# Optimization experiments

Hardware: AMD Instinct MI355X
Metric: run time of the kernel (lower is better)

## Reference

```python
import jax, jax.numpy as jnp
import numpy as np

HEADS = 8
NEG_SLOPE = 0.2  # PyG GATConv default LeakyReLU slope


def _gat_layer(x, src, dst, W, a_src, a_dst, bias, heads, out_ch):
    """PyG-style GATConv (concat heads, self-loops already appended, eval mode).
    x: [N, F_in]; src/dst: [E_tot] int; W: [F_in, heads*out_ch];
    a_src/a_dst: [heads, out_ch]; bias: [heads*out_ch].
    """
    N = x.shape[0]
    h = (x @ W).reshape(N, heads, out_ch)                      # [N, H, C]
    # per-node attention logits (gathered per edge as scalars, not features)
    al_s = jnp.einsum('nhc,hc->nh', h, a_src)                  # [N, H]
    al_d = jnp.einsum('nhc,hc->nh', h, a_dst)                  # [N, H]
    e = jax.nn.leaky_relu(al_s[src] + al_d[dst], negative_slope=NEG_SLOPE)  # [E, H]
    # segment softmax over incoming edges of each target node (stable)
    e_max = jax.ops.segment_max(e, dst, num_segments=N)        # self-loops => no empty segments
    ex = jnp.exp(e - e_max[dst])
    denom = jax.ops.segment_sum(ex, dst, num_segments=N)
    alpha = ex / (denom[dst] + 1e-16)                          # [E, H]
    # gather source features, weight, scatter-add to targets
    out = jax.ops.segment_sum(h[src] * alpha[:, :, None], dst, num_segments=N)  # [N, H, C]
    return out.reshape(N, heads * out_ch) + bias


def setup_inputs() -> dict:
    key = jax.random.key(0)
    ks = jax.random.split(key, 16)
    N, E, F_IN, NUM_CLASSES = 50000, 1600000, 128, 16
    s = 0.1
    return {
        'x': jax.random.normal(ks[0], (N, F_IN), dtype=jnp.float32),
        'edge_index': jax.random.randint(ks[1], (2, E), 0, N, dtype=jnp.int64),
        # GAT layer 1: 128 -> 8 heads x 8
        'W1': jax.random.normal(ks[2], (F_IN, 64), dtype=jnp.float32) * s,
        'a1_src': jax.random.normal(ks[3], (8, 8), dtype=jnp.float32) * s,
        'a1_dst': jax.random.normal(ks[4], (8, 8), dtype=jnp.float32) * s,
        'b1': jnp.zeros((64,), dtype=jnp.float32),
        # GAT layer 2: 64 -> 8 heads x 4
        'W2': jax.random.normal(ks[5], (64, 32), dtype=jnp.float32) * s,
        'a2_src': jax.random.normal(ks[6], (8, 4), dtype=jnp.float32) * s,
        'a2_dst': jax.random.normal(ks[7], (8, 4), dtype=jnp.float32) * s,
        'b2': jnp.zeros((32,), dtype=jnp.float32),
        # torch MultiheadAttention(32, 8): packed in_proj [96,32], out_proj [32,32]
        'in_proj_w': jax.random.normal(ks[8], (96, 32), dtype=jnp.float32) * s,
        'in_proj_b': jnp.zeros((96,), dtype=jnp.float32),
        'out_proj_w': jax.random.normal(ks[9], (32, 32), dtype=jnp.float32) * s,
        'out_proj_b': jnp.zeros((32,), dtype=jnp.float32),
        # fc: 32 -> num_classes
        'fc_w': jax.random.normal(ks[10], (NUM_CLASSES, 32), dtype=jnp.float32) * s,
        'fc_b': jnp.zeros((NUM_CLASSES,), dtype=jnp.float32),
    }


def reference(x, edge_index, W1, a1_src, a1_dst, b1, W2, a2_src, a2_dst, b2,
              in_proj_w, in_proj_b, out_proj_w, out_proj_b, fc_w, fc_b):
    N = x.shape[0]
    loops = jnp.arange(N, dtype=edge_index.dtype)
    src = jnp.concatenate([edge_index[0], loops])  # PyG add_self_loops=True
    dst = jnp.concatenate([edge_index[1], loops])

    h = jax.nn.elu(_gat_layer(x, src, dst, W1, a1_src, a1_dst, b1, HEADS, 8))   # [N, 64]
    h = jax.nn.elu(_gat_layer(h, src, dst, W2, a2_src, a2_dst, b2, HEADS, 4))   # [N, 32]

    # MultiheadAttention on h.unsqueeze(0): shape [1, N, 32] with torch's
    # seq-first layout => seq_len = 1, batch = N. Softmax over a single key
    # is identically 1 for every head, so out = out_proj(v_proj(h)).
    v = h @ in_proj_w[64:96].T + in_proj_b[64:96]   # v-projection slice of packed in_proj
    h = v @ out_proj_w.T + out_proj_b               # [N, 32]

    logits = h @ fc_w.T + fc_b                      # [N, num_classes]
    return jax.nn.log_softmax(logits, axis=1)
```

## Files before the change

kernel.cpp:

```cpp
#include <hip/hip_runtime.h>
#include <hip/hip_bf16.h>
#include <math.h>


#define BSHIFT 7
#define BMASK  ((1 << BSHIFT) - 1)
#define MAXNB  512
#define TILE   8192
#define XST    136
#define SMBYTES 36864

typedef __attribute__((ext_vector_type(8))) short short8;
typedef __attribute__((ext_vector_type(4))) float floatx4;
typedef __attribute__((ext_vector_type(2))) float floatx2;

__device__ __forceinline__ unsigned short f2bf(float f) {
    union { float f; unsigned int u; } v; v.f = f;
    unsigned int u = v.u;
    return (unsigned short)((u + 0x7FFFu + ((u >> 16) & 1u)) >> 16);
}
__device__ __forceinline__ float lrelu(float e) { return fmaxf(e, 0.2f * e); }
__device__ __forceinline__ float elu(float o) {
    return (o > 0.f) ? o : (__expf(o) - 1.f);
}

__global__ __launch_bounds__(256) void fused_pre_kernel(
    const float* __restrict__ x, const float* __restrict__ W,
    const float* __restrict__ a_src, const float* __restrict__ a_dst,
    char* __restrict__ rec1, float* __restrict__ ald, int N, int GB,
    const int* __restrict__ ei, int E, int Et, int NB, int CAP,
    int* __restrict__ gcount, unsigned int* __restrict__ rec, int NT,
    const float* __restrict__ in_proj_w, const float* __restrict__ in_proj_b,
    const float* __restrict__ out_proj_w, const float* __restrict__ out_proj_b,
    const float* __restrict__ fc_w, const float* __restrict__ fc_b,
    float* __restrict__ M, float* __restrict__ bf) {
    __shared__ __align__(16) char sm[SMBYTES];
    int t = threadIdx.x;
    int bid = blockIdx.x;
    if (bid < GB) {
        unsigned short* xs = (unsigned short*)sm;
        unsigned short* wt = xs + 64 * XST;
        int nb = bid * 64;
#pragma unroll
        for (int r = 0; r < 8; ++r) {
            int p = t + 256 * r;
            int row = p >> 5;
            int c4  = p & 31;
            int n = nb + row;
            float4 v = (n < N) ? ((const float4*)x)[(size_t)n * 32 + c4]
                               : make_float4(0.f, 0.f, 0.f, 0.f);
            unsigned short* dst = &xs[row * XST + c4 * 4];
            dst[0] = f2bf(v.x); dst[1] = f2bf(v.y);
            dst[2] = f2bf(v.z); dst[3] = f2bf(v.w);
        }
        {
            int n = t & 63, kg = t >> 6;
#pragma unroll
            for (int c = 0; c < 4; ++c) {
                int k0 = kg * 32 + c * 8;
                unsigned short* dst = &wt[n * XST + k0];
#pragma unroll
                for (int j = 0; j < 8; ++j)
                    dst[j] = f2bf(W[(k0 + j) * 64 + n]);
            }
        }
        __syncthreads();
        int wave = t >> 6, lane = t & 63;
        int m16 = lane & 15, quad = lane >> 4;
        floatx4 acc[4];
#pragma unroll
        for (int i = 0; i < 4; ++i) acc[i] = (floatx4){0.f, 0.f, 0.f, 0.f};
#pragma unroll
        for (int k = 0; k < 4; ++k) {
            int koff = k * 32 + quad * 8;
            short8 afrag = *(const short8*)&xs[(wave * 16 + m16) * XST + koff];
#pragma unroll
            for (int nt = 0; nt < 4; ++nt) {
                short8 bfrag = *(const short8*)&wt[(nt * 16 + m16) * XST + koff];
                acc[nt] = __builtin_amdgcn_mfma_f32_16x16x32_bf16(afrag, bfrag, acc[nt], 0, 0, 0);
            }
        }
        __syncthreads();
        float* hs = (float*)sm;
#pragma unroll
        for (int nt = 0; nt < 4; ++nt)
#pragma unroll
            for (int r = 0; r < 4; ++r)
                hs[(wave * 16 + quad * 4 + r) * 65 + nt * 16 + m16] = acc[nt][r];
        __syncthreads();
        float asv = a_src[lane], adv = a_dst[lane];
        for (int itn = 0; itn < 16; ++itn) {
            int nl = wave * 16 + itn;
            int n = nb + nl;
            if (n >= N) break;
            float v = hs[nl * 65 + lane];
            float ps = v * asv, pd = v * adv;
            ps += __shfl_xor(ps, 1); ps += __shfl_xor(ps, 2); ps += __shfl_xor(ps, 4);
            pd += __shfl_xor(pd, 1); pd += __shfl_xor(pd, 2); pd += __shfl_xor(pd, 4);
            if ((lane & 7) == 0) {
                *(float*)(rec1 + (size_t)n * 128 + 4 * (lane >> 3)) = ps;
                ald[n * 8 + (lane >> 3)] = pd;
            }
            if (lane < 16) {
                const float* hr = &hs[nl * 65 + lane * 4];
                int pk = __builtin_amdgcn_cvt_pk_fp8_f32(hr[0], hr[1], 0, false);
                pk = __builtin_amdgcn_cvt_pk_fp8_f32(hr[2], hr[3], pk, true);
                *(unsigned*)(rec1 + (size_t)n * 128 + 64 + 4 * lane) = (unsigned)pk;
            }
        }
    } else if (bid < GB + NT) {
        unsigned int* lrec = (unsigned int*)sm;
        int* h   = (int*)(sm + TILE * 4);
        int* cur = (int*)(sm + TILE * 4 + MAXNB * 4);
        for (int i = t; i < NB; i += 256) h[i] = 0;
        int tile0 = (bid - GB) * TILE;
        int cnt = Et - tile0; if (cnt > TILE) cnt = TILE;
        __syncthreads();
        for (int j = t; j < cnt; j += 256) {
            int jj = tile0 + j;
            int srcv, d;
            if (jj < E) { srcv = ei[jj]; d = ei[E + jj]; } else { srcv = jj - E; d = jj - E; }
            lrec[j] = (unsigned)srcv | ((unsigned)d << 16);
            atomicAdd(&h[d >> BSHIFT], 1);
        }
        __syncthreads();
        for (int i = t; i < NB; i += 256)
            cur[i] = h[i] ? atomicAdd(&gcount[i], h[i]) : 0;
        __syncthreads();
        for (int j = t; j < cnt; j += 256) {
            unsigned v = lrec[j];
            int b = v >> (16 + BSHIFT);
            int pos = atomicAdd(&cur[b], 1);
            if (pos < CAP)
                rec[(size_t)b * CAP + pos] =
                    (v & 0xFFFFu) | ((((v >> 16) & BMASK)) << 16);
        }
    } else {
        float* Wvo = (float*)sm;
        float* bvo = (float*)(sm + 4096);
        const float* Wv = in_proj_w + 64 * 32;
        const float* bv = in_proj_b + 64;
        for (int idx = t; idx < 1024; idx += 256) {
            int i = idx >> 5, j = idx & 31;
            float acc = 0.f;
            for (int k = 0; k < 32; ++k) acc += out_proj_w[i * 32 + k] * Wv[k * 32 + j];
            Wvo[idx] = acc;
        }
        if (t < 32) {
            float acc = 0.f;
            for (int k = 0; k < 32; ++k) acc += out_proj_w[t * 32 + k] * bv[k];
            bvo[t] = acc + out_proj_b[t];
        }
        __syncthreads();
        for (int idx = t; idx < 16 * 32; idx += 256) {
            int cc = idx >> 5, j = idx & 31;
            float acc = 0.f;
            for (int i = 0; i < 32; ++i) acc += fc_w[cc * 32 + i] * Wvo[i * 32 + j];
            M[idx] = acc;
        }
        if (t < 16) {
            float acc = 0.f;
            for (int i = 0; i < 32; ++i) acc += fc_w[t * 32 + i] * bvo[i];
            bf[t] = acc + fc_b[t];
        }
    }
}

__global__ __launch_bounds__(256) void csr_finalize_kernel(
    const unsigned int* __restrict__ rec, const int* __restrict__ gcount,
    int* __restrict__ rowp, unsigned short* __restrict__ esrc,
    int N, int Et, int CAP) {
    __shared__ int h[128];
    __shared__ int nb[128];
    __shared__ int cur[128];
    __shared__ int ssum[256];
    int b = blockIdx.x, t = threadIdx.x;
    size_t rbase = (size_t)b * CAP;
    int cnt = gcount[b]; if (cnt > CAP) cnt = CAP;
    if (t < 128) h[t] = 0;
    int acc = 0;
    for (int i = t; i < b; i += 256) {
        int v = gcount[i];
        acc += (v < CAP) ? v : CAP;
    }
    ssum[t] = acc;
    __syncthreads();
    for (int off = 128; off >= 1; off >>= 1) {
        if (t < off) ssum[t] += ssum[t + off];
        __syncthreads();
    }
    int obase = ssum[0];
    for (int i = t; i < cnt; i += 256)
        atomicAdd(&h[(rec[rbase + i] >> 16) & 127], 1);
    __syncthreads();
    if (t == 0) {
        int run = obase;
        for (int i = 0; i < 128; ++i) { nb[i] = run; run += h[i]; }
    }
    __syncthreads();
    if (t < 128) cur[t] = nb[t];
    int n0 = b << BSHIFT;
    if (t < 128 && n0 + t < N) rowp[n0 + t] = nb[t];
    if (b == 0 && t == 0) rowp[N] = Et;
    __syncthreads();
    for (int i = t; i < cnt; i += 256) {
        unsigned r = rec[rbase + i];
        int pos = atomicAdd(&cur[(r >> 16) & 127], 1);
        esrc[pos] = (unsigned short)(r & 0xFFFFu);
    }
}

__global__ __launch_bounds__(256) void gat_agg64_g2_kernel(
    const int* __restrict__ rowp, const unsigned short* __restrict__ esrc,
    const char* __restrict__ rec1, const float* __restrict__ ald_arr,
    const float* __restrict__ bias,
    const float* __restrict__ W2, const float* __restrict__ a2s,
    const float* __restrict__ a2d,
    char* __restrict__ rec2, float* __restrict__ ald2, int N) {
    __shared__ __align__(16) float W2p[2][8][32][4];
    __shared__ __align__(16) float oL[4][64];
    __shared__ __align__(16) float h2L[4][32];
    int t = threadIdx.x;
    for (int idx = t; idx < 2048; idx += 256) {
        int k = idx >> 5, l = idx & 31;
        W2p[k >> 5][(k & 31) >> 2][l][k & 3] = W2[idx];
    }
    __syncthreads();
    const int lane = t & 63;
    const int wv = t >> 6;
    const int e = lane >> 4;
    const int c = lane & 15;
    const int hd = c >> 1;
    const int aoff = 4 * hd;
    const int foff = 64 + 4 * c;
    int n = blockIdx.x * 4 + wv;
    if (n >= N) return;
    float aldv = ald_arr[n * 8 + hd];
    int beg = rowp[n], end = rowp[n + 1];
    float dA = 0.f, dB = 0.f;
    floatx2 p0a = {0.f, 0.f}, p0b = {0.f, 0.f};
    floatx2 p1a = {0.f, 0.f}, p1b = {0.f, 0.f};
    floatx2 p2a = {0.f, 0.f}, p2b = {0.f, 0.f};
    floatx2 p3a = {0.f, 0.f}, p3b = {0.f, 0.f};
    int i = beg;
    for (; i + 32 <= end; i += 32) {
        int s0 = esrc[i + e],      s1 = esrc[i + 4 + e];
        int s2 = esrc[i + 8 + e],  s3 = esrc[i + 12 + e];
        int s4 = esrc[i + 16 + e], s5 = esrc[i + 20 + e];
        int s6 = esrc[i + 24 + e], s7 = esrc[i + 28 + e];
        const char* r0 = rec1 + (size_t)s0 * 128;
        const char* r1 = rec1 + (size_t)s1 * 128;
        const char* r2 = rec1 + (size_t)s2 * 128;
        const char* r3 = rec1 + (size_t)s3 * 128;
        const char* r4 = rec1 + (size_t)s4 * 128;
        const char* r5 = rec1 + (size_t)s5 * 128;
        const char* r6 = rec1 + (size_t)s6 * 128;
        const char* r7 = rec1 + (size_t)s7 * 128;
        float e0 = *(const float*)(r0 + aoff), e1 = *(const float*)(r1 + aoff);
        float e2 = *(const float*)(r2 + aoff), e3 = *(const float*)(r3 + aoff);
        float e4 = *(const float*)(r4 + aoff), e5 = *(const float*)(r5 + aoff);
        float e6 = *(const float*)(r6 + aoff), e7 = *(const float*)(r7 + aoff);
        unsigned g0 = *(const unsigned*)(r0 + foff), g1 = *(const unsigned*)(r1 + foff);
        unsigned g2 = *(const unsigned*)(r2 + foff), g3 = *(const unsigned*)(r3 + foff);
        unsigned g4 = *(const unsigned*)(r4 + foff), g5 = *(const unsigned*)(r5 + foff);
        unsigned g6 = *(const unsigned*)(r6 + foff), g7 = *(const unsigned*)(r7 + foff);
        float w0 = __expf(lrelu(e0 + aldv));
        float w1 = __expf(lrelu(e1 + aldv));
        float w2 = __expf(lrelu(e2 + aldv));
        float w3 = __expf(lrelu(e3 + aldv));
        float w4 = __expf(lrelu(e4 + aldv));
        float w5 = __expf(lrelu(e5 + aldv));
        float w6 = __expf(lrelu(e6 + aldv));
        float w7 = __expf(lrelu(e7 + aldv));
        dA += w0 + w2; dB += w1 + w3;
        dA += w4 + w6; dB += w5 + w7;
        p0a += w0 * __builtin_amdgcn_cvt_pk_f32_fp8(g0, false);
        p0b += w0 * __builtin_amdgcn_cvt_pk_f32_fp8(g0, true);
        p1a += w1 * __builtin_amdgcn_cvt_pk_f32_fp8(g1, false);
        p1b += w1 * __builtin_amdgcn_cvt_pk_f32_fp8(g1, true);
        p2a += w2 * __builtin_amdgcn_cvt_pk_f32_fp8(g2, false);
        p2b += w2 * __builtin_amdgcn_cvt_pk_f32_fp8(g2, true);
        p3a += w3 * __builtin_amdgcn_cvt_pk_f32_fp8(g3, false);
        p3b += w3 * __builtin_amdgcn_cvt_pk_f32_fp8(g3, true);
        p0a += w4 * __builtin_amdgcn_cvt_pk_f32_fp8(g4, false);
        p0b += w4 * __builtin_amdgcn_cvt_pk_f32_fp8(g4, true);
        p1a += w5 * __builtin_amdgcn_cvt_pk_f32_fp8(g5, false);
        p1b += w5 * __builtin_amdgcn_cvt_pk_f32_fp8(g5, true);
        p2a += w6 * __builtin_amdgcn_cvt_pk_f32_fp8(g6, false);
        p2b += w6 * __builtin_amdgcn_cvt_pk_f32_fp8(g6, true);
        p3a += w7 * __builtin_amdgcn_cvt_pk_f32_fp8(g7, false);
        p3b += w7 * __builtin_amdgcn_cvt_pk_f32_fp8(g7, true);
    }
    for (; i < end; i += 16) {
        int i0 = i + e, i1 = i + 4 + e, i2 = i + 8 + e, i3 = i + 12 + e;
        bool v0 = i0 < end, v1 = i1 < end, v2 = i2 < end, v3 = i3 < end;
        int c0 = v0 ? i0 : beg;
        int c1 = v1 ? i1 : beg;
        int c2 = v2 ? i2 : beg;
        int c3 = v3 ? i3 : beg;
        int s0 = esrc[c0], s1 = esrc[c1], s2 = esrc[c2], s3 = esrc[c3];
        const char* r0 = rec1 + (size_t)s0 * 128;
        const char* r1 = rec1 + (size_t)s1 * 128;
        const char* r2 = rec1 + (size_t)s2 * 128;
        const char* r3 = rec1 + (size_t)s3 * 128;
        float e0 = *(const float*)(r0 + aoff), e1 = *(const float*)(r1 + aoff);
        float e2 = *(const float*)(r2 + aoff), e3 = *(const float*)(r3 + aoff);
        unsigned g0 = *(const unsigned*)(r0 + foff), g1 = *(const unsigned*)(r1 + foff);
        unsigned g2 = *(const unsigned*)(r2 + foff), g3 = *(const unsigned*)(r3 + foff);
        float w0 = v0 ? __expf(lrelu(e0 + aldv)) : 0.f;
        float w1 = v1 ? __expf(lrelu(e1 + aldv)) : 0.f;
        float w2 = v2 ? __expf(lrelu(e2 + aldv)) : 0.f;
        float w3 = v3 ? __expf(lrelu(e3 + aldv)) : 0.f;
        dA += w0 + w2; dB += w1 + w3;
        p0a += w0 * __builtin_amdgcn_cvt_pk_f32_fp8(g0, false);
        p0b += w0 * __builtin_amdgcn_cvt_pk_f32_fp8(g0, true);
        p1a += w1 * __builtin_amdgcn_cvt_pk_f32_fp8(g1, false);
        p1b += w1 * __builtin_amdgcn_cvt_pk_f32_fp8(g1, true);
        p2a += w2 * __builtin_amdgcn_cvt_pk_f32_fp8(g2, false);
        p2b += w2 * __builtin_amdgcn_cvt_pk_f32_fp8(g2, true);
        p3a += w3 * __builtin_amdgcn_cvt_pk_f32_fp8(g3, false);
        p3b += w3 * __builtin_amdgcn_cvt_pk_f32_fp8(g3, true);
    }
    float d = dA + dB;
    floatx2 Pa = (p0a + p1a) + (p2a + p3a);
    floatx2 Pb = (p0b + p1b) + (p2b + p3b);
    float P0 = Pa.x, P1 = Pa.y, P2 = Pb.x, P3 = Pb.y;
    d  += __shfl_xor(d, 16);  d  += __shfl_xor(d, 32);
    P0 += __shfl_xor(P0, 16); P0 += __shfl_xor(P0, 32);
    P1 += __shfl_xor(P1, 16); P1 += __shfl_xor(P1, 32);
    P2 += __shfl_xor(P2, 16); P2 += __shfl_xor(P2, 32);
    P3 += __shfl_xor(P3, 16); P3 += __shfl_xor(P3, 32);
    float inv = 1.f / (d + 1e-16f);
    float4 bv = ((const float4*)bias)[c];
    float o0 = elu(P0 * inv + bv.x);
    float o1 = elu(P1 * inv + bv.y);
    float o2 = elu(P2 * inv + bv.z);
    float o3 = elu(P3 * inv + bv.w);
    if (lane < 16) *(float4*)&oL[wv][c * 4] = make_float4(o0, o1, o2, o3);
    const int l = lane & 31, kh = lane >> 5;
    const float* orow = &oL[wv][kh * 32];
    float a0 = 0.f, a1 = 0.f, a2 = 0.f, a3 = 0.f;
#pragma unroll
    for (int g = 0; g < 8; ++g) {
        float4 ov = *(const float4*)&orow[g * 4];
        float4 wv4 = *(const float4*)&W2p[kh][g][l][0];
        a0 += ov.x * wv4.x; a1 += ov.y * wv4.y;
        a2 += ov.z * wv4.z; a3 += ov.w * wv4.w;
    }
    float acc = (a0 + a1) + (a2 + a3);
    acc += __shfl_xor(acc, 32);
    float ps = acc * a2s[l], pd = acc * a2d[l];
    ps += __shfl_xor(ps, 1); ps += __shfl_xor(ps, 2);
    pd += __shfl_xor(pd, 1); pd += __shfl_xor(pd, 2);
    if (lane < 32) {
        h2L[wv][l] = acc;
        if ((l & 3) == 0) {
            *(float*)(rec2 + (size_t)n * 64 + 4 * (l >> 2)) = ps;
            ald2[n * 8 + (l >> 2)] = pd;
        }
    }
    if (lane < 8) {
        const float* hr = &h2L[wv][lane * 4];
        int pk = __builtin_amdgcn_cvt_pk_fp8_f32(hr[0], hr[1], 0, false);
        pk = __builtin_amdgcn_cvt_pk_fp8_f32(hr[2], hr[3], pk, true);
        *(unsigned*)(rec2 + (size_t)n * 64 + 32 + 4 * lane) = (unsigned)pk;
    }
}

__global__ __launch_bounds__(256) void gat_agg32_fin_kernel(
    const int* __restrict__ rowp, const unsigned short* __restrict__ esrc,
    const char* __restrict__ rec2, const float* __restrict__ ald_arr,
    const float* __restrict__ bias,
    const float* __restrict__ M, const float* __restrict__ bf,
    float* __restrict__ out, int N) {
    __shared__ __align__(16) float Mp[8][16][4];
    __shared__ float bfs[16];
    __shared__ __align__(16) float oL[4][32];
    int t = threadIdx.x;
    for (int i = t; i < 512; i += 256) {
        int j = i >> 5, k = i & 31;
        Mp[k >> 2][j][k & 3] = M[i];
    }
    if (t < 16) bfs[t] = bf[t];
    __syncthreads();
    const int lane = t & 63;
    const int wv = t >> 6;
    const int e = lane >> 3;
    const int c = lane & 7;
    const int aoff = 4 * c;
    const int foff = 32 + 4 * c;
    int n = blockIdx.x * 4 + wv;
    if (n >= N) return;
    float aldv = ald_arr[n * 8 + c];
    int beg = rowp[n], end = rowp[n + 1];
    float d0 = 0.f, d1 = 0.f, d2 = 0.f, d3 = 0.f;
    floatx2 p0a = {0.f, 0.f}, p0b = {0.f, 0.f};
    floatx2 p1a = {0.f, 0.f}, p1b = {0.f, 0.f};
    floatx2 p2a = {0.f, 0.f}, p2b = {0.f, 0.f};
    floatx2 p3a = {0.f, 0.f}, p3b = {0.f, 0.f};
    int base = beg;
    for (; base + 32 <= end; base += 32) {
        int s0 = esrc[base + e],      s1 = esrc[base + 8 + e];
        int s2 = esrc[base + 16 + e], s3 = esrc[base + 24 + e];
        const char* r0 = rec2 + (size_t)s0 * 64;
        const char* r1 = rec2 + (size_t)s1 * 64;
        const char* r2 = rec2 + (size_t)s2 * 64;
        const char* r3 = rec2 + (size_t)s3 * 64;
        float e0 = *(const float*)(r0 + aoff) + aldv;
        float e1 = *(const float*)(r1 + aoff) + aldv;
        float e2 = *(const float*)(r2 + aoff) + aldv;
        float e3 = *(const float*)(r3 + aoff) + aldv;
        unsigned g0 = *(const unsigned*)(r0 + foff);
        unsigned g1 = *(const unsigned*)(r1 + foff);
        unsigned g2 = *(const unsigned*)(r2 + foff);
        unsigned g3 = *(const unsigned*)(r3 + foff);
        float w0 = __expf(lrelu(e0));
        float w1 = __expf(lrelu(e1));
        float w2 = __expf(lrelu(e2));
        float w3 = __expf(lrelu(e3));
        d0 += w0; d1 += w1; d2 += w2; d3 += w3;
        p0a += w0 * __builtin_amdgcn_cvt_pk_f32_fp8(g0, false);
        p0b += w0 * __builtin_amdgcn_cvt_pk_f32_fp8(g0, true);
        p1a += w1 * __builtin_amdgcn_cvt_pk_f32_fp8(g1, false);
        p1b += w1 * __builtin_amdgcn_cvt_pk_f32_fp8(g1, true);
        p2a += w2 * __builtin_amdgcn_cvt_pk_f32_fp8(g2, false);
        p2b += w2 * __builtin_amdgcn_cvt_pk_f32_fp8(g2, true);
        p3a += w3 * __builtin_amdgcn_cvt_pk_f32_fp8(g3, false);
        p3b += w3 * __builtin_amdgcn_cvt_pk_f32_fp8(g3, true);
    }
    for (; base < end; base += 32) {
        int i0 = base + e;
        int i1 = base + 8 + e;
        int i2 = base + 16 + e;
        int i3 = base + 24 + e;
        bool v0 = i0 < end, v1 = i1 < end, v2 = i2 < end, v3 = i3 < end;
        int c0 = v0 ? i0 : beg;
        int c1 = v1 ? i1 : beg;
        int c2 = v2 ? i2 : beg;
        int c3 = v3 ? i3 : beg;
        int s0 = esrc[c0], s1 = esrc[c1], s2 = esrc[c2], s3 = esrc[c3];
        const char* r0 = rec2 + (size_t)s0 * 64;
        const char* r1 = rec2 + (size_t)s1 * 64;
        const char* r2 = rec2 + (size_t)s2 * 64;
        const char* r3 = rec2 + (size_t)s3 * 64;
        float e0 = *(const float*)(r0 + aoff) + aldv;
        float e1 = *(const float*)(r1 + aoff) + aldv;
        float e2 = *(const float*)(r2 + aoff) + aldv;
        float e3 = *(const float*)(r3 + aoff) + aldv;
        unsigned g0 = *(const unsigned*)(r0 + foff);
        unsigned g1 = *(const unsigned*)(r1 + foff);
        unsigned g2 = *(const unsigned*)(r2 + foff);
        unsigned g3 = *(const unsigned*)(r3 + foff);
        float w0 = v0 ? __expf(lrelu(e0)) : 0.f;
        float w1 = v1 ? __expf(lrelu(e1)) : 0.f;
        float w2 = v2 ? __expf(lrelu(e2)) : 0.f;
        float w3 = v3 ? __expf(lrelu(e3)) : 0.f;
        d0 += w0; d1 += w1; d2 += w2; d3 += w3;
        p0a += w0 * __builtin_amdgcn_cvt_pk_f32_fp8(g0, false);
        p0b += w0 * __builtin_amdgcn_cvt_pk_f32_fp8(g0, true);
        p1a += w1 * __builtin_amdgcn_cvt_pk_f32_fp8(g1, false);
        p1b += w1 * __builtin_amdgcn_cvt_pk_f32_fp8(g1, true);
        p2a += w2 * __builtin_amdgcn_cvt_pk_f32_fp8(g2, false);
        p2b += w2 * __builtin_amdgcn_cvt_pk_f32_fp8(g2, true);
        p3a += w3 * __builtin_amdgcn_cvt_pk_f32_fp8(g3, false);
        p3b += w3 * __builtin_amdgcn_cvt_pk_f32_fp8(g3, true);
    }
    float d = (d0 + d1) + (d2 + d3);
    floatx2 Pa = (p0a + p1a) + (p2a + p3a);
    floatx2 Pb = (p0b + p1b) + (p2b + p3b);
    float P0 = Pa.x, P1 = Pa.y, P2 = Pb.x, P3 = Pb.y;
    d  += __shfl_xor(d, 8);  d  += __shfl_xor(d, 16);  d  += __shfl_xor(d, 32);
    P0 += __shfl_xor(P0, 8); P0 += __shfl_xor(P0, 16); P0 += __shfl_xor(P0, 32);
    P1 += __shfl_xor(P1, 8); P1 += __shfl_xor(P1, 16); P1 += __shfl_xor(P1, 32);
    P2 += __shfl_xor(P2, 8); P2 += __shfl_xor(P2, 16); P2 += __shfl_xor(P2, 32);
    P3 += __shfl_xor(P3, 8); P3 += __shfl_xor(P3, 16); P3 += __shfl_xor(P3, 32);
    float inv = 1.f / (d + 1e-16f);
    float4 bv = ((const float4*)bias)[c];
    float o0 = elu(P0 * inv + bv.x);
    float o1 = elu(P1 * inv + bv.y);
    float o2 = elu(P2 * inv + bv.z);
    float o3 = elu(P3 * inv + bv.w);
    if (lane < 8) *(float4*)&oL[wv][c * 4] = make_float4(o0, o1, o2, o3);
    const int j = lane & 15;
    const float* orow = oL[wv];
    float a0 = 0.f, a1 = 0.f, a2 = 0.f, a3 = 0.f;
#pragma unroll
    for (int g = 0; g < 8; ++g) {
        float4 ov = *(const float4*)&orow[g * 4];
        float4 mv = *(const float4*)&Mp[g][j][0];
        a0 += ov.x * mv.x; a1 += ov.y * mv.y;
        a2 += ov.z * mv.z; a3 += ov.w * mv.w;
    }
    float logit = (a0 + a1) + (a2 + a3) + bfs[j];
    float mx = logit;
    mx = fmaxf(mx, __shfl_xor(mx, 1));
    mx = fmaxf(mx, __shfl_xor(mx, 2));
    mx = fmaxf(mx, __shfl_xor(mx, 4));
    mx = fmaxf(mx, __shfl_xor(mx, 8));
    float ex = __expf(logit - mx);
    float se = ex;
    se += __shfl_xor(se, 1);
    se += __shfl_xor(se, 2);
    se += __shfl_xor(se, 4);
    se += __shfl_xor(se, 8);
    float res = logit - (mx + __logf(se));
    if (lane < 16) out[(size_t)n * 16 + j] = res;
}

extern "C" void kernel_launch(void* const* d_in, const int* in_sizes, int n_in,
                              void* d_out, int out_size, void* d_ws, size_t ws_size,
                              hipStream_t stream) {
    const float* x   = (const float*)d_in[0];
    const int*   ei  = (const int*)d_in[1];
    const float* W1  = (const float*)d_in[2];
    const float* a1s = (const float*)d_in[3];
    const float* a1d = (const float*)d_in[4];
    const float* b1  = (const float*)d_in[5];
    const float* W2  = (const float*)d_in[6];
    const float* a2s = (const float*)d_in[7];
    const float* a2d = (const float*)d_in[8];
    const float* b2  = (const float*)d_in[9];
    const float* ipw = (const float*)d_in[10];
    const float* ipb = (const float*)d_in[11];
    const float* opw = (const float*)d_in[12];
    const float* opb = (const float*)d_in[13];
    const float* fcw = (const float*)d_in[14];
    const float* fcb = (const float*)d_in[15];
    float* out = (float*)d_out;

    int N = in_sizes[0] / 128;
    int E = in_sizes[1] / 2;
    int Et = E + N;
    int NB = (N + BMASK) >> BSHIFT;
    int NTILES = (Et + TILE - 1) / TILE;
    int GB = (N + 63) / 64;
    int CAP = Et / NB;
    CAP = CAP + CAP / 8 + 256;
    CAP = (CAP + 255) & ~255;

    char* ws = (char*)d_ws;
    size_t off = 0;
    auto alloc = [&](size_t bytes) -> void* {
        void* p = ws + off;
        off += bytes;
        off = (off + 255) & ~(size_t)255;
        return p;
    };
    int*   bcount = (int*)alloc(MAXNB * 4);
    unsigned int*   rec  = (unsigned int*)alloc((size_t)NB * CAP * 4);
    int*   rowp   = (int*)alloc((size_t)(N + 1) * 4);
    unsigned short* esrc = (unsigned short*)alloc((size_t)Et * 2);
    char* rec1   = (char*)alloc((size_t)N * 128);
    float* al1d  = (float*)alloc((size_t)N * 8 * 4);
    char* rec2   = (char*)alloc((size_t)N * 64);
    float* al2d  = (float*)alloc((size_t)N * 8 * 4);
    float* Mf    = (float*)alloc(512 * 4);
    float* bff   = (float*)alloc(16 * 4);
    (void)ws_size; (void)n_in; (void)out_size;

    hipMemsetAsync(bcount, 0, MAXNB * 4, stream);
    fused_pre_kernel<<<GB + NTILES + 1, 256, 0, stream>>>(
        x, W1, a1s, a1d, rec1, al1d, N, GB,
        ei, E, Et, NB, CAP, bcount, rec, NTILES,
        ipw, ipb, opw, opb, fcw, fcb, Mf, bff);
    csr_finalize_kernel<<<NB, 256, 0, stream>>>(rec, bcount, rowp, esrc, N, Et, CAP);

    gat_agg64_g2_kernel<<<(N + 3) / 4, 256, 0, stream>>>(
        rowp, esrc, rec1, al1d, b1, W2, a2s, a2d, rec2, al2d, N);
    gat_agg32_fin_kernel<<<(N + 3) / 4, 256, 0, stream>>>(
        rowp, esrc, rec2, al2d, b2, Mf, bff, out, N);
}
```

Before: 211.9 us.

## Stage CSR scatter in LDS and widen per-lane feature loads in layer-1 aggregation

The CSR finalize kernel now scatters each bucket's edge sources into a shared-memory buffer and then writes them to global memory contiguously, replacing random global scatter writes. CAP is clamped to the LDS buffer size, which could drop edges if a bucket overflows. The layer-1 aggregation kernel remaps lanes so each lane handles one full head (8 fp8 features via a 64-bit load) across 8 edge slots, instead of half a head across 4 slots. This gives fewer, wider gathers per edge and one attention exp per head-edge, at the cost of an extra shuffle stage and more accumulators.

```diff
diff --git a/kernel.cpp b/kernel.cpp
--- a/kernel.cpp
+++ b/kernel.cpp
@@ -9,6 +9,7 @@
 #define TILE   8192
 #define XST    136
 #define SMBYTES 36864
+#define LESRC_MAX 6144
 
 typedef __attribute__((ext_vector_type(8))) short short8;
 typedef __attribute__((ext_vector_type(4))) float floatx4;
@@ -174,6 +175,7 @@
     __shared__ int nb[128];
     __shared__ int cur[128];
     __shared__ int ssum[256];
+    __shared__ unsigned short lesrc[LESRC_MAX];
     int b = blockIdx.x, t = threadIdx.x;
     size_t rbase = (size_t)b * CAP;
     int cnt = gcount[b]; if (cnt > CAP) cnt = CAP;
@@ -194,20 +196,23 @@
         atomicAdd(&h[(rec[rbase + i] >> 16) & 127], 1);
     __syncthreads();
     if (t == 0) {
-        int run = obase;
+        int run = 0;
         for (int i = 0; i < 128; ++i) { nb[i] = run; run += h[i]; }
     }
     __syncthreads();
     if (t < 128) cur[t] = nb[t];
     int n0 = b << BSHIFT;
-    if (t < 128 && n0 + t < N) rowp[n0 + t] = nb[t];
+    if (t < 128 && n0 + t < N) rowp[n0 + t] = obase + nb[t];
     if (b == 0 && t == 0) rowp[N] = Et;
     __syncthreads();
     for (int i = t; i < cnt; i += 256) {
         unsigned r = rec[rbase + i];
         int pos = atomicAdd(&cur[(r >> 16) & 127], 1);
-        esrc[pos] = (unsigned short)(r & 0xFFFFu);
-    }
+        lesrc[pos] = (unsigned short)(r & 0xFFFFu);
+    }
+    __syncthreads();
+    for (int i = t; i < cnt; i += 256)
+        esrc[obase + i] = lesrc[i];
 }
 
 __global__ __launch_bounds__(256) void gat_agg64_g2_kernel(
@@ -228,71 +233,53 @@
     __syncthreads();
     const int lane = t & 63;
     const int wv = t >> 6;
-    const int e = lane >> 4;
-    const int c = lane & 15;
-    const int hd = c >> 1;
-    const int aoff = 4 * hd;
-    const int foff = 64 + 4 * c;
+    const int e = lane >> 3;
+    const int c = lane & 7;
+    const int aoff = 4 * c;
+    const int foff = 64 + 8 * c;
     int n = blockIdx.x * 4 + wv;
     if (n >= N) return;
-    float aldv = ald_arr[n * 8 + hd];
+    float aldv = ald_arr[n * 8 + c];
     int beg = rowp[n], end = rowp[n + 1];
     float dA = 0.f, dB = 0.f;
-    floatx2 p0a = {0.f, 0.f}, p0b = {0.f, 0.f};
-    floatx2 p1a = {0.f, 0.f}, p1b = {0.f, 0.f};
-    floatx2 p2a = {0.f, 0.f}, p2b = {0.f, 0.f};
-    floatx2 p3a = {0.f, 0.f}, p3b = {0.f, 0.f};
+    floatx2 A0 = {0.f, 0.f}, A1 = {0.f, 0.f}, A2 = {0.f, 0.f}, A3 = {0.f, 0.f};
+    floatx2 B0 = {0.f, 0.f}, B1 = {0.f, 0.f}, B2 = {0.f, 0.f}, B3 = {0.f, 0.f};
     int i = beg;
     for (; i + 32 <= end; i += 32) {
-        int s0 = esrc[i + e],      s1 = esrc[i + 4 + e];
-        int s2 = esrc[i + 8 + e],  s3 = esrc[i + 12 + e];
-        int s4 = esrc[i + 16 + e], s5 = esrc[i + 20 + e];
-        int s6 = esrc[i + 24 + e], s7 = esrc[i + 28 + e];
+        int s0 = esrc[i + e],      s1 = esrc[i + 8 + e];
+        int s2 = esrc[i + 16 + e], s3 = esrc[i + 24 + e];
         const char* r0 = rec1 + (size_t)s0 * 128;
         const char* r1 = rec1 + (size_t)s1 * 128;
         const char* r2 = rec1 + (size_t)s2 * 128;
         const char* r3 = rec1 + (size_t)s3 * 128;
-        const char* r4 = rec1 + (size_t)s4 * 128;
-        const char* r5 = rec1 + (size_t)s5 * 128;
-        const char* r6 = rec1 + (size_t)s6 * 128;
-        const char* r7 = rec1 + (size_t)s7 * 128;
         float e0 = *(const float*)(r0 + aoff), e1 = *(const float*)(r1 + aoff);
         float e2 = *(const float*)(r2 + aoff), e3 = *(const float*)(r3 + aoff);
-        float e4 = *(const float*)(r4 + aoff), e5 = *(const float*)(r5 + aoff);
-        float e6 = *(const float*)(r6 + aoff), e7 = *(const float*)(r7 + aoff);
-        unsigned g0 = *(const unsigned*)(r0 + foff), g1 = *(const unsigned*)(r1 + foff);
-        unsigned g2 = *(const unsigned*)(r2 + foff), g3 = *(const unsigned*)(r3 + foff);
-        unsigned g4 = *(const unsigned*)(r4 + foff), g5 = *(const unsigned*)(r5 + foff);
-        unsigned g6 = *(const unsigned*)(r6 + foff), g7 = *(const unsigned*)(r7 + foff);
+        uint2 g0 = *(const uint2*)(r0 + foff), g1 = *(const uint2*)(r1 + foff);
+        uint2 g2 = *(const uint2*)(r2 + foff), g3 = *(const uint2*)(r3 + foff);
         float w0 = __expf(lrelu(e0 + aldv));
         float w1 = __expf(lrelu(e1 + aldv));
         float w2 = __expf(lrelu(e2 + aldv));
         float w3 = __expf(lrelu(e3 + aldv));
-        float w4 = __expf(lrelu(e4 + aldv));
-        float w5 = __expf(lrelu(e5 + aldv));
-        float w6 = __expf(lrelu(e6 + aldv));
-        float w7 = __expf(lrelu(e7 + aldv));
         dA += w0 + w2; dB += w1 + w3;
-        dA += w4 + w6; dB += w5 + w7;
-        p0a += w0 * __builtin_amdgcn_cvt_pk_f32_fp8(g0, false);
-        p0b += w0 * __builtin_amdgcn_cvt_pk_f32_fp8(g0, true);
-        p1a += w1 * __builtin_amdgcn_cvt_pk_f32_fp8(g1, false);
-        p1b += w1 * __builtin_amdgcn_cvt_pk_f32_fp8(g1, true);
-        p2a += w2 * __builtin_amdgcn_cvt_pk_f32_fp8(g2, false);
-        p2b += w2 * __builtin_amdgcn_cvt_pk_f32_fp8(g2, true);
-        p3a += w3 * __builtin_amdgcn_cvt_pk_f32_fp8(g3, false);
-        p3b += w3 * __builtin_amdgcn_cvt_pk_f32_fp8(g3, true);
-        p0a += w4 * __builtin_amdgcn_cvt_pk_f32_fp8(g4, false);
-        p0b += w4 * __builtin_amdgcn_cvt_pk_f32_fp8(g4, true);
-        p1a += w5 * __builtin_amdgcn_cvt_pk_f32_fp8(g5, false);
-        p1b += w5 * __builtin_amdgcn_cvt_pk_f32_fp8(g5, true);
-        p2a += w6 * __builtin_amdgcn_cvt_pk_f32_fp8(g6, false);
-        p2b += w6 * __builtin_amdgcn_cvt_pk_f32_fp8(g6, true);
-        p3a += w7 * __builtin_amdgcn_cvt_pk_f32_fp8(g7, false);
-        p3b += w7 * __builtin_amdgcn_cvt_pk_f32_fp8(g7, true);
-    }
-    for (; i < end; i += 16) {
-        int i0 = i + e, i1 = i + 4 + e, i2 = i + 8 + e, i3 = i + 12 + e;
+        A0 += w0 * __builtin_amdgcn_cvt_pk_f32_fp8(g0.x, false);
+        A1 += w0 * __builtin_amdgcn_cvt_pk_f32_fp8(g0.x, true);
+        A2 += w0 * __builtin_amdgcn_cvt_pk_f32_fp8(g0.y, false);
+        A3 += w0 * __builtin_amdgcn_cvt_pk_f32_fp8(g0.y, true);
+        B0 += w1 * __builtin_amdgcn_cvt_pk_f32_fp8(g1.x, false);
+        B1 += w1 * __builtin_amdgcn_cvt_pk_f32_fp8(g1.x, true);
+        B2 += w1 * __builtin_amdgcn_cvt_pk_f32_fp8(g1.y, false);
+        B3 += w1 * __builtin_amdgcn_cvt_pk_f32_fp8(g1.y, true);
+        A0 += w2 * __builtin_amdgcn_cvt_pk_f32_fp8(g2.x, false);
+        A1 += w2 * __builtin_amdgcn_cvt_pk_f32_fp8(g2.x, true);
+        A2 += w2 * __builtin_amdgcn_cvt_pk_f32_fp8(g2.y, false);
+        A3 += w2 * __builtin_amdgcn_cvt_pk_f32_fp8(g2.y, true);
+        B0 += w3 * __builtin_amdgcn_cvt_pk_f32_fp8(g3.x, false);
+        B1 += w3 * __builtin_amdgcn_cvt_pk_f32_fp8(g3.x, true);
+        B2 += w3 * __builtin_amdgcn_cvt_pk_f32_fp8(g3.y, false);
+        B3 += w3 * __builtin_amdgcn_cvt_pk_f32_fp8(g3.y, true);
+    }
+    for (; i < end; i += 32) {
+        int i0 = i + e, i1 = i + 8 + e, i2 = i + 16 + e, i3 = i + 24 + e;
         bool v0 = i0 < end, v1 = i1 < end, v2 = i2 < end, v3 = i3 < end;
         int c0 = v0 ? i0 : beg;
         int c1 = v1 ? i1 : beg;
@@ -305,38 +292,59 @@
         const char* r3 = rec1 + (size_t)s3 * 128;
         float e0 = *(const float*)(r0 + aoff), e1 = *(const float*)(r1 + aoff);
         float e2 = *(const float*)(r2 + aoff), e3 = *(const float*)(r3 + aoff);
-        unsigned g0 = *(const unsigned*)(r0 + foff), g1 = *(const unsigned*)(r1 + foff);
-        unsigned g2 = *(const unsigned*)(r2 + foff), g3 = *(const unsigned*)(r3 + foff);
+        uint2 g0 = *(const uint2*)(r0 + foff), g1 = *(const uint2*)(r1 + foff);
+        uint2 g2 = *(const uint2*)(r2 + foff), g3 = *(const uint2*)(r3 + foff);
         float w0 = v0 ? __expf(lrelu(e0 + aldv)) : 0.f;
         float w1 = v1 ? __expf(lrelu(e1 + aldv)) : 0.f;
         float w2 = v2 ? __expf(lrelu(e2 + aldv)) : 0.f;
         float w3 = v3 ? __expf(lrelu(e3 + aldv)) : 0.f;
         dA += w0 + w2; dB += w1 + w3;
-        p0a += w0 * __builtin_amdgcn_cvt_pk_f32_fp8(g0, false);
-        p0b += w0 * __builtin_amdgcn_cvt_pk_f32_fp8(g0, true);
-        p1a += w1 * __builtin_amdgcn_cvt_pk_f32_fp8(g1, false);
-        p1b += w1 * __builtin_amdgcn_cvt_pk_f32_fp8(g1, true);
-        p2a += w2 * __builtin_amdgcn_cvt_pk_f32_fp8(g2, false);
-        p2b += w2 * __builtin_amdgcn_cvt_pk_f32_fp8(g2, true);
-        p3a += w3 * __builtin_amdgcn_cvt_pk_f32_fp8(g3, false);
-        p3b += w3 * __builtin_amdgcn_cvt_pk_f32_fp8(g3, true);
+        A0 += w0 * __builtin_amdgcn_cvt_pk_f32_fp8(g0.x, false);
+        A1 += w0 * __builtin_amdgcn_cvt_pk_f32_fp8(g0.x, true);
+        A2 += w0 * __builtin_amdgcn_cvt_pk_f32_fp8(g0.y, false);
+        A3 += w0 * __builtin_amdgcn_cvt_pk_f32_fp8(g0.y, true);
+        B0 += w1 * __builtin_amdgcn_cvt_pk_f32_fp8(g1.x, false);
+        B1 += w1 * __builtin_amdgcn_cvt_pk_f32_fp8(g1.x, true);
+        B2 += w1 * __builtin_amdgcn_cvt_pk_f32_fp8(g1.y, false);
+        B3 += w1 * __builtin_amdgcn_cvt_pk_f32_fp8(g1.y, true);
+        A0 += w2 * __builtin_amdgcn_cvt_pk_f32_fp8(g2.x, false);
+        A1 += w2 * __builtin_amdgcn_cvt_pk_f32_fp8(g2.x, true);
+        A2 += w2 * __builtin_amdgcn_cvt_pk_f32_fp8(g2.y, false);
+        A3 += w2 * __builtin_amdgcn_cvt_pk_f32_fp8(g2.y, true);
+        B0 += w3 * __builtin_amdgcn_cvt_pk_f32_fp8(g3.x, false);
+        B1 += w3 * __builtin_amdgcn_cvt_pk_f32_fp8(g3.x, true);
+        B2 += w3 * __builtin_amdgcn_cvt_pk_f32_fp8(g3.y, false);
+        B3 += w3 * __builtin_amdgcn_cvt_pk_f32_fp8(g3.y, true);
     }
     float d = dA + dB;
-    floatx2 Pa = (p0a + p1a) + (p2a + p3a);
-    floatx2 Pb = (p0b + p1b) + (p2b + p3b);
-    float P0 = Pa.x, P1 = Pa.y, P2 = Pb.x, P3 = Pb.y;
-    d  += __shfl_xor(d, 16);  d  += __shfl_xor(d, 32);
-    P0 += __shfl_xor(P0, 16); P0 += __shfl_xor(P0, 32);
-    P1 += __shfl_xor(P1, 16); P1 += __shfl_xor(P1, 32);
-    P2 += __shfl_xor(P2, 16); P2 += __shfl_xor(P2, 32);
-    P3 += __shfl_xor(P3, 16); P3 += __shfl_xor(P3, 32);
+    float P0 = A0.x + B0.x, P1 = A0.y + B0.y;
+    float P2 = A1.x + B1.x, P3 = A1.y + B1.y;
+    float P4 = A2.x + B2.x, P5 = A2.y + B2.y;
+    float P6 = A3.x + B3.x, P7 = A3.y + B3.y;
+    d  += __shfl_xor(d, 8);  d  += __shfl_xor(d, 16);  d  += __shfl_xor(d, 32);
+    P0 += __shfl_xor(P0, 8); P0 += __shfl_xor(P0, 16); P0 += __shfl_xor(P0, 32);
+    P1 += __shfl_xor(P1, 8); P1 += __shfl_xor(P1, 16); P1 += __shfl_xor(P1, 32);
+    P2 += __shfl_xor(P2, 8); P2 += __shfl_xor(P2, 16); P2 += __shfl_xor(P2, 32);
+    P3 += __shfl_xor(P3, 8); P3 += __shfl_xor(P3, 16); P3 += __shfl_xor(P3, 32);
+    P4 += __shfl_xor(P4, 8); P4 += __shfl_xor(P4, 16); P4 += __shfl_xor(P4, 32);
+    P5 += __shfl_xor(P5, 8); P5 += __shfl_xor(P5, 16); P5 += __shfl_xor(P5, 32);
+    P6 += __shfl_xor(P6, 8); P6 += __shfl_xor(P6, 16); P6 += __shfl_xor(P6, 32);
+    P7 += __shfl_xor(P7, 8); P7 += __shfl_xor(P7, 16); P7 += __shfl_xor(P7, 32);
     float inv = 1.f / (d + 1e-16f);
-    float4 bv = ((const float4*)bias)[c];
-    float o0 = elu(P0 * inv + bv.x);
-    float o1 = elu(P1 * inv + bv.y);
-    float o2 = elu(P2 * inv + bv.z);
-    float o3 = elu(P3 * inv + bv.w);
-    if (lane < 16) *(float4*)&oL[wv][c * 4] = make_float4(o0, o1, o2, o3);
+    float4 bv0 = ((const float4*)bias)[2 * c];
+    float4 bv1 = ((const float4*)bias)[2 * c + 1];
+    float o0 = elu(P0 * inv + bv0.x);
+    float o1 = elu(P1 * inv + bv0.y);
+    float o2 = elu(P2 * inv + bv0.z);
+    float o3 = elu(P3 * inv + bv0.w);
+    float o4 = elu(P4 * inv + bv1.x);
+    float o5 = elu(P5 * inv + bv1.y);
+    float o6 = elu(P6 * inv + bv1.z);
+    float o7 = elu(P7 * inv + bv1.w);
+    if (lane < 8) {
+        *(float4*)&oL[wv][c * 8]     = make_float4(o0, o1, o2, o3);
+        *(float4*)&oL[wv][c * 8 + 4] = make_float4(o4, o5, o6, o7);
+    }
     const int l = lane & 31, kh = lane >> 5;
     const float* orow = &oL[wv][kh * 32];
     float a0 = 0.f, a1 = 0.f, a2 = 0.f, a3 = 0.f;
@@ -537,6 +545,7 @@
     int CAP = Et / NB;
     CAP = CAP + CAP / 8 + 256;
     CAP = (CAP + 255) & ~255;
+    if (CAP > LESRC_MAX) CAP = LESRC_MAX;
 
     char* ws = (char*)d_ws;
     size_t off = 0;
```

After: 212.3 us. No clear change (+0.2%).
